# Performance work log

Hardware: AMD Instinct MI355X
Metric: run time of the kernel (lower is better)

## Reference

```python
import jax, jax.numpy as jnp
import numpy as np

EPS = 1e-8


def quaternion_mul(q, m):
    # Hamilton product q * m over last dim of size 4 (w, x, y, z)
    w1, x1, y1, z1 = q[..., 0], q[..., 1], q[..., 2], q[..., 3]
    w2, x2, y2, z2 = m[..., 0], m[..., 1], m[..., 2], m[..., 3]
    return jnp.stack([
        w1 * w2 - x1 * x2 - y1 * y2 - z1 * z2,
        w1 * x2 + x1 * w2 + y1 * z2 - z1 * y2,
        w1 * y2 - x1 * z2 + y1 * w2 + z1 * x2,
        w1 * z2 + x1 * y2 - y1 * x2 + z1 * w2,
    ], axis=-1)


def quaternion_normalize(q):
    n = jnp.linalg.norm(q, axis=-1, keepdims=True)
    return q / (n + EPS)


def setup_inputs() -> dict:
    key = jax.random.key(0)
    k = jax.random.split(key, 5)
    B, S, D, H = 4, 2048, 1024, 1024
    scale = 0.02
    return {
        "x": jax.random.normal(k[0], (B, S, D), dtype=jnp.float32),
        "W_in": jax.random.normal(k[1], (3 * H, D), dtype=jnp.float32) * scale,
        "b_in": jax.random.normal(k[2], (3 * H,), dtype=jnp.float32) * scale,
        "W_out": jax.random.normal(k[3], (D, 4 * H), dtype=jnp.float32) * scale,
        "b_out": jax.random.normal(k[4], (D,), dtype=jnp.float32) * scale,
    }


def reference(x, W_in, b_in, W_out, b_out):
    B, S, D = x.shape
    H = W_in.shape[0] // 3
    # input projection -> rotation parameters v in R^3 per hidden channel
    v = (jnp.einsum('bsd,ed->bse', x, W_in) + b_in).reshape(B, S, H, 3)
    # SU(2) exponential map: v -> unit quaternion
    theta = jnp.linalg.norm(v, axis=-1, keepdims=True)          # (B,S,H,1)
    axis = v / (theta + EPS)
    q_inputs = jnp.concatenate([jnp.cos(theta), jnp.sin(theta) * axis], axis=-1)  # (B,S,H,4)

    # initial identity quaternion state (B,H,4)
    m0 = jnp.zeros((B, H, 4), dtype=x.dtype).at[..., 0].set(1.0)

    def step(m, q_t):
        m_new = quaternion_normalize(quaternion_mul(q_t, m))
        return m_new, m_new

    q_seq = jnp.transpose(q_inputs, (1, 0, 2, 3))               # (S,B,H,4)
    m_final, ms = jax.lax.scan(step, m0, q_seq)                 # ms: (S,B,H,4)

    states = jnp.transpose(ms, (1, 0, 2, 3)).reshape(B, S, 4 * H)
    full_output = jnp.einsum('bsf,df->bsd', states, W_out) + b_out
    return full_output, m_final
```

## Files before the change

kernel.cpp:

```cpp
#include <hip/hip_runtime.h>
#include <hip/hip_bf16.h>
#include <stdint.h>

#define EPSF 1e-8f

typedef __attribute__((ext_vector_type(8))) short short8;
typedef __attribute__((ext_vector_type(8))) _Float16 half8;
typedef __attribute__((ext_vector_type(4))) float floatx4;

__device__ __forceinline__ unsigned short f2h(float f) {
    _Float16 h = (_Float16)f;
    return __builtin_bit_cast(unsigned short, h);
}
__device__ __forceinline__ float h2f(unsigned short u) {
    return (float)__builtin_bit_cast(_Float16, u);
}


__global__ void prep_kernel(const float4* __restrict__ x4, ushort4* __restrict__ x16,
                            const float4* __restrict__ wi4, ushort4* __restrict__ wi16,
                            const float4* __restrict__ wo4, ushort4* __restrict__ wo16,
                            int nx4, int nw4, int nwo4) {
    int i = blockIdx.x * blockDim.x + threadIdx.x;
    float4 f; ushort4 u;
    if (i < nx4) {
        f = x4[i];
        u.x = f2h(f.x); u.y = f2h(f.y); u.z = f2h(f.z); u.w = f2h(f.w);
        x16[i] = u;
    } else if (i < nx4 + nw4) {
        int j = i - nx4;
        f = wi4[j];
        u.x = f2h(f.x); u.y = f2h(f.y); u.z = f2h(f.z); u.w = f2h(f.w);
        wi16[j] = u;
    } else if (i < nx4 + nw4 + nwo4) {
        int j = i - nx4 - nw4;
        f = wo4[j];
        u.x = f2h(f.x); u.y = f2h(f.y); u.z = f2h(f.z); u.w = f2h(f.w);
        wo16[j] = u;
    }
}


__device__ __forceinline__ void gld16(const unsigned short* g, unsigned short* l) {
    __builtin_amdgcn_global_load_lds(
        (const __attribute__((address_space(1))) unsigned int*)g,
        (__attribute__((address_space(3))) unsigned int*)l, 16, 0, 0);
}

template <bool HALFOUT>
__global__ __launch_bounds__(512, 2)
void gemm8p(const unsigned short* __restrict__ Am, const unsigned short* __restrict__ Bm,
            const float* __restrict__ bias, void* __restrict__ Cv,
            int M, int N, int K) {
    constexpr int BM = 256, BN = 128, BK = 64;
    constexpr int ASZ  = BM * BK;
    constexpr int BSZ  = BN * BK;
    constexpr int SLOT = ASZ + BSZ;
    extern __shared__ unsigned short smem[];

    const int tid  = threadIdx.x;
    const int lane = tid & 63;
    const int wid  = tid >> 6;
    const int wr   = wid >> 1;
    const int wc   = wid & 1;
    const int q4   = lane >> 4;
    const int m16  = lane & 15;
    const int x7   = m16 & 7;

    const int nbx = N / BN;
    const int nwg = gridDim.x;
    const int q   = nwg >> 3;
    const int wg  = blockIdx.x;
    const int sz  = (wg & 7) * q + (wg >> 3);
    const int bx  = sz % nbx, by = sz / nbx;
    const int rowA0 = by * BM, rowB0 = bx * BN;

    const int rA = tid >> 3, cA = tid & 7;
    const int cg = cA ^ (rA & 7);
    const unsigned short* srcA = Am + (size_t)(rowA0 + rA) * K + cg * 8;
    const unsigned short* srcB = Bm + (size_t)(rowB0 + rA) * K + cg * 8;
    const int dA = tid * 8;

    int aoffm[4], boffn[4];
#pragma unroll
    for (int m = 0; m < 4; ++m) aoffm[m] = (wr * 64 + m * 16 + m16) * BK;
#pragma unroll
    for (int n = 0; n < 4; ++n) boffn[n] = (wc * 64 + n * 16 + m16) * BK;

    floatx4 acc[4][4];
#pragma unroll
    for (int m = 0; m < 4; ++m)
#pragma unroll
        for (int n = 0; n < 4; ++n)
#pragma unroll
            for (int r = 0; r < 4; ++r) acc[m][n][r] = 0.f;

    const int NT = K / BK;

    auto stageA = [&](int s, int t, int j) {
        gld16(srcA + (size_t)(j * 64) * K + (size_t)t * BK,
              smem + s * SLOT + j * 4096 + dA);
    };
    auto stageB = [&](int s, int t, int j) {
        gld16(srcB + (size_t)(j * 64) * K + (size_t)t * BK,
              smem + s * SLOT + ASZ + j * 4096 + dA);
    };

#pragma unroll
    for (int j = 0; j < 4; ++j) stageA(0, 0, j);
    stageB(0, 0, 0); stageB(0, 0, 1);
#pragma unroll
    for (int j = 0; j < 4; ++j) stageA(1, 1, j);
    stageB(1, 1, 0); stageB(1, 1, 1);

    int s0 = 0;
    for (int t = 0; t < NT; ++t) {
        int s2 = s0 + 2; if (s2 >= 3) s2 -= 3;
        if (t + 1 < NT) asm volatile("s_waitcnt vmcnt(6)" ::: "memory");
        else            asm volatile("s_waitcnt vmcnt(0)" ::: "memory");
        __builtin_amdgcn_s_barrier();
        __builtin_amdgcn_sched_barrier(0);

        const unsigned short* tA = smem + s0 * SLOT;
        const unsigned short* tB = tA + ASZ;

        if (t + 2 < NT) {
#pragma unroll
            for (int j = 0; j < 4; ++j) stageA(s2, t + 2, j);
            stageB(s2, t + 2, 0); stageB(s2, t + 2, 1);
        }

        short8 a0[4], b0[4], a1[4], b1[4];
        {
            const int xo = ((0 + q4) ^ x7) * 8;
#pragma unroll
            for (int m = 0; m < 4; ++m) a0[m] = *(const short8*)(tA + aoffm[m] + xo);
#pragma unroll
            for (int n = 0; n < 4; ++n) b0[n] = *(const short8*)(tB + boffn[n] + xo);
        }
        __builtin_amdgcn_s_setprio(1);
#pragma unroll
        for (int m = 0; m < 4; ++m)
#pragma unroll
            for (int n = 0; n < 4; ++n)
                acc[m][n] = __builtin_amdgcn_mfma_f32_16x16x32_f16(
                    __builtin_bit_cast(half8, a0[m]), __builtin_bit_cast(half8, b0[n]),
                    acc[m][n], 0, 0, 0);
        __builtin_amdgcn_s_setprio(0);

        {
            const int xo = ((4 + q4) ^ x7) * 8;
#pragma unroll
            for (int m = 0; m < 4; ++m) a1[m] = *(const short8*)(tA + aoffm[m] + xo);
#pragma unroll
            for (int n = 0; n < 4; ++n) b1[n] = *(const short8*)(tB + boffn[n] + xo);
        }
        __builtin_amdgcn_s_setprio(1);
#pragma unroll
        for (int m = 0; m < 4; ++m)
#pragma unroll
            for (int n = 0; n < 4; ++n)
                acc[m][n] = __builtin_amdgcn_mfma_f32_16x16x32_f16(
                    __builtin_bit_cast(half8, a1[m]), __builtin_bit_cast(half8, b1[n]),
                    acc[m][n], 0, 0, 0);
        __builtin_amdgcn_s_setprio(0);

        s0 = (s0 + 1 == 3) ? 0 : s0 + 1;
    }

#pragma unroll
    for (int m = 0; m < 4; ++m) {
#pragma unroll
        for (int n = 0; n < 4; ++n) {
            int col  = rowB0 + wc * 64 + n * 16 + m16;
            float bvl = bias[col];
#pragma unroll
            for (int r = 0; r < 4; ++r) {
                int row = rowA0 + wr * 64 + m * 16 + q4 * 4 + r;
                if (HALFOUT)
                    ((unsigned short*)Cv)[(size_t)row * N + col] = f2h(acc[m][n][r] + bvl);
                else
                    ((float*)Cv)[(size_t)row * N + col] = acc[m][n][r] + bvl;
            }
        }
    }
}


struct Q { float w, x, y, z; };

__device__ __forceinline__ Q qmul(Q a, Q b) {
    Q r;
    r.w = a.w * b.w - a.x * b.x - a.y * b.y - a.z * b.z;
    r.x = a.w * b.x + a.x * b.w + a.y * b.z - a.z * b.y;
    r.y = a.w * b.y - a.x * b.z + a.y * b.w + a.z * b.x;
    r.z = a.w * b.z + a.x * b.y - a.y * b.x + a.z * b.w;
    return r;
}
__device__ __forceinline__ Q qnorm(Q a) {
    float nn = a.w * a.w + a.x * a.x + a.y * a.y + a.z * a.z;
    float inv = __frsqrt_rn(nn);
    Q r; r.w = a.w * inv; r.x = a.x * inv; r.y = a.y * inv; r.z = a.z * inv;
    return r;
}
__device__ __forceinline__ Q vquat(float vx, float vy, float vz) {
    float th = sqrtf(vx * vx + vy * vy + vz * vz);
    float s_, c_;
    __sincosf(th, &s_, &c_);
    float k = __fdividef(s_, th + EPSF);
    Q q; q.w = c_; q.x = k * vx; q.y = k * vy; q.z = k * vz;
    return q;
}

#define SEG  64
#define NSEG 32

__global__ __launch_bounds__(256)
void seg_prod_kernel(const unsigned short* __restrict__ v, float* __restrict__ partials,
                     int S, int H) {
    const int b  = blockIdx.z;
    const int h  = blockIdx.y * 64 + (threadIdx.x & 63);
    const int sg = blockIdx.x * 4 + (threadIdx.x >> 6);
    const int s0 = sg * SEG;
    const size_t vstep = (size_t)3 * H;
    const unsigned short* vp = v + ((size_t)b * S + s0) * vstep + (size_t)h * 3;

    constexpr int CH = 8;
    float ax[CH], ay[CH], az[CH], bx[CH], by[CH], bz[CH];
#pragma unroll
    for (int i = 0; i < CH; ++i) {
        ax[i] = h2f(vp[i * vstep + 0]); ay[i] = h2f(vp[i * vstep + 1]); az[i] = h2f(vp[i * vstep + 2]);
    }
    Q c = {1.f, 0.f, 0.f, 0.f};
    const int NC = SEG / CH;
    for (int cc = 0; cc < NC; cc += 2) {
        if (cc + 1 < NC) {
            const unsigned short* p = vp + (size_t)(cc + 1) * CH * vstep;
#pragma unroll
            for (int i = 0; i < CH; ++i) {
                bx[i] = h2f(p[i * vstep + 0]); by[i] = h2f(p[i * vstep + 1]); bz[i] = h2f(p[i * vstep + 2]);
            }
        }
#pragma unroll
        for (int i = 0; i < CH; ++i) c = qmul(vquat(ax[i], ay[i], az[i]), c);
        if (cc + 2 < NC) {
            const unsigned short* p = vp + (size_t)(cc + 2) * CH * vstep;
#pragma unroll
            for (int i = 0; i < CH; ++i) {
                ax[i] = h2f(p[i * vstep + 0]); ay[i] = h2f(p[i * vstep + 1]); az[i] = h2f(p[i * vstep + 2]);
            }
        }
#pragma unroll
        for (int i = 0; i < CH; ++i) c = qmul(vquat(bx[i], by[i], bz[i]), c);
    }
    float4* dst = (float4*)(partials + (((size_t)b * NSEG + sg) * H + h) * 4);
    *dst = make_float4(c.w, c.x, c.y, c.z);
}

__global__ __launch_bounds__(256)
void apply_kernel(const unsigned short* __restrict__ v, const float* __restrict__ partials,
                  unsigned short* __restrict__ st, float* __restrict__ m_final,
                  int S, int H) {
    const int b   = blockIdx.z;
    const int hb  = blockIdx.y * 64;
    const int hl  = threadIdx.x & 63;
    const int h   = hb + hl;
    const int sg  = blockIdx.x * 4 + (threadIdx.x >> 6);
    const int s0  = sg * SEG;
    const size_t vstep = (size_t)3 * H;
    const size_t sstep = (size_t)4 * H;
    const unsigned short* vp = v + ((size_t)b * S + s0) * vstep + (size_t)h * 3;
    unsigned short* sp = st + ((size_t)b * S + s0) * sstep + (size_t)h * 4;

    __shared__ float4 lp[NSEG][64];
    for (int i = threadIdx.x; i < NSEG * 64; i += 256) {
        int s2 = i >> 6, hh = i & 63;
        lp[s2][hh] = *(const float4*)(partials + (((size_t)b * NSEG + s2) * H + hb + hh) * 4);
    }
    __syncthreads();

    Q R = {1.f, 0.f, 0.f, 0.f};
    for (int s2 = 0; s2 < sg; ++s2) {
        float4 pv = lp[s2][hl];
        Q pq = {pv.x, pv.y, pv.z, pv.w};
        R = qmul(pq, R);
    }

    constexpr int CH = 8;
    float ax[CH], ay[CH], az[CH], bx[CH], by[CH], bz[CH];
#pragma unroll
    for (int i = 0; i < CH; ++i) {
        ax[i] = h2f(vp[i * vstep + 0]); ay[i] = h2f(vp[i * vstep + 1]); az[i] = h2f(vp[i * vstep + 2]);
    }
    const int NC = SEG / CH;
    for (int cc = 0; cc < NC; cc += 2) {
        if (cc + 1 < NC) {
            const unsigned short* pp = vp + (size_t)(cc + 1) * CH * vstep;
#pragma unroll
            for (int i = 0; i < CH; ++i) {
                bx[i] = h2f(pp[i * vstep + 0]); by[i] = h2f(pp[i * vstep + 1]); bz[i] = h2f(pp[i * vstep + 2]);
            }
        }
#pragma unroll
        for (int i = 0; i < CH; ++i) {
            R = qmul(vquat(ax[i], ay[i], az[i]), R);
            Q m = qnorm(R);
            ushort4 u; u.x = f2h(m.w); u.y = f2h(m.x); u.z = f2h(m.y); u.w = f2h(m.z);
            *(ushort4*)(sp + (size_t)(cc * CH + i) * sstep) = u;
        }
        if (cc + 2 < NC) {
            const unsigned short* pp = vp + (size_t)(cc + 2) * CH * vstep;
#pragma unroll
            for (int i = 0; i < CH; ++i) {
                ax[i] = h2f(pp[i * vstep + 0]); ay[i] = h2f(pp[i * vstep + 1]); az[i] = h2f(pp[i * vstep + 2]);
            }
        }
#pragma unroll
        for (int i = 0; i < CH; ++i) {
            R = qmul(vquat(bx[i], by[i], bz[i]), R);
            Q m = qnorm(R);
            ushort4 u; u.x = f2h(m.w); u.y = f2h(m.x); u.z = f2h(m.y); u.w = f2h(m.z);
            *(ushort4*)(sp + (size_t)((cc + 1) * CH + i) * sstep) = u;
        }
    }

    if (sg == NSEG - 1) {
        Q m = qnorm(R);
        float* mf = m_final + ((size_t)b * H + h) * 4;
        mf[0] = m.w; mf[1] = m.x; mf[2] = m.y; mf[3] = m.z;
    }
}


extern "C" void kernel_launch(void* const* d_in, const int* in_sizes, int n_in,
                              void* d_out, int out_size, void* d_ws, size_t ws_size,
                              hipStream_t stream) {
    const float* x     = (const float*)d_in[0];
    const float* W_in  = (const float*)d_in[1];
    const float* b_in  = (const float*)d_in[2];
    const float* W_out = (const float*)d_in[3];
    const float* b_out = (const float*)d_in[4];
    float* out = (float*)d_out;

    const int B = 4, S = 2048, D = 1024, H = 1024;
    const int M  = B * S;
    const int N1 = 3 * H;
    const int K1 = D;
    const int N2 = D;
    const int K2 = 4 * H;

    char* ws = (char*)d_ws;
    unsigned short* v    = (unsigned short*)(ws);
    unsigned short* st   = (unsigned short*)(ws + 50331648u);
    unsigned short* x16  = (unsigned short*)(ws + 50331648u);
    unsigned short* wi16 = (unsigned short*)(ws + 50331648u + 16777216u);
    unsigned short* wo16 = (unsigned short*)(ws + 117440512u);

    float* partials = out;

    const int nx  = M * K1;
    const int nw  = N1 * K1;
    const int nwo = N2 * K2;
    const int n4  = (nx + nw + nwo) / 4;

    constexpr int LDSB = 147456;
    static int attr_done = 0;
    if (!attr_done) {
        hipFuncSetAttribute(reinterpret_cast<const void*>(&gemm8p<true>),
                            hipFuncAttributeMaxDynamicSharedMemorySize, LDSB);
        hipFuncSetAttribute(reinterpret_cast<const void*>(&gemm8p<false>),
                            hipFuncAttributeMaxDynamicSharedMemorySize, LDSB);
        attr_done = 1;
    }

    prep_kernel<<<(n4 + 255) / 256, 256, 0, stream>>>(
        (const float4*)x, (ushort4*)x16, (const float4*)W_in, (ushort4*)wi16,
        (const float4*)W_out, (ushort4*)wo16, nx / 4, nw / 4, nwo / 4);

    gemm8p<true><<<dim3((M / 256) * (N1 / 128)), 512, LDSB, stream>>>(
        x16, wi16, b_in, v, M, N1, K1);

    dim3 sg_grid(NSEG / 4, H / 64, B);
    seg_prod_kernel<<<sg_grid, 256, 0, stream>>>(v, partials, S, H);
    apply_kernel<<<sg_grid, 256, 0, stream>>>(v, partials, st, out + (size_t)M * D, S, H);

    gemm8p<false><<<dim3((M / 256) * (N2 / 128)), 512, LDSB, stream>>>(
        st, wo16, b_out, out, M, N2, K2);
}
```

Measured before the change: 297.4 us.

## Switch GEMM to 32x32x16 MFMA with software-pipelined LDS fragment reads

Replaces the 16x16x32 MFMA tiling (4x4 accumulators per wave) with 32x32x16 MFMA instructions (2x2 accumulators of 16 floats). The main loop is restructured so LDS fragment reads for the next k-slice, including the first slice of the next tile, are issued before the MFMAs on the current slice. The barrier/waitcnt placement moves to mid-iteration to allow this prefetch. The aim is fewer LDS reads per FLOP and better overlap of LDS latency with matrix math. The cost is more complex synchronisation and a different output row mapping in the epilogue.

```diff
diff --git a/kernel.cpp b/kernel.cpp
--- a/kernel.cpp
+++ b/kernel.cpp
@@ -6,7 +6,7 @@
 
 typedef __attribute__((ext_vector_type(8))) short short8;
 typedef __attribute__((ext_vector_type(8))) _Float16 half8;
-typedef __attribute__((ext_vector_type(4))) float floatx4;
+typedef __attribute__((ext_vector_type(16))) float floatx16;
 
 __device__ __forceinline__ unsigned short f2h(float f) {
     _Float16 h = (_Float16)f;
@@ -63,9 +63,9 @@
     const int wid  = tid >> 6;
     const int wr   = wid >> 1;
     const int wc   = wid & 1;
-    const int q4   = lane >> 4;
-    const int m16  = lane & 15;
-    const int x7   = m16 & 7;
+    const int m32  = lane & 31;
+    const int half = lane >> 5;
+    const int x7   = m32 & 7;
 
     const int nbx = N / BN;
     const int nwg = gridDim.x;
@@ -81,19 +81,19 @@
     const unsigned short* srcB = Bm + (size_t)(rowB0 + rA) * K + cg * 8;
     const int dA = tid * 8;
 
-    int aoffm[4], boffn[4];
-#pragma unroll
-    for (int m = 0; m < 4; ++m) aoffm[m] = (wr * 64 + m * 16 + m16) * BK;
-#pragma unroll
-    for (int n = 0; n < 4; ++n) boffn[n] = (wc * 64 + n * 16 + m16) * BK;
-
-    floatx4 acc[4][4];
-#pragma unroll
-    for (int m = 0; m < 4; ++m)
-#pragma unroll
-        for (int n = 0; n < 4; ++n)
-#pragma unroll
-            for (int r = 0; r < 4; ++r) acc[m][n][r] = 0.f;
+    int aoff[2], boff[2];
+#pragma unroll
+    for (int m = 0; m < 2; ++m) aoff[m] = (wr * 64 + m * 32 + m32) * BK;
+#pragma unroll
+    for (int n = 0; n < 2; ++n) boff[n] = (wc * 64 + n * 32 + m32) * BK;
+
+    floatx16 acc[2][2];
+#pragma unroll
+    for (int m = 0; m < 2; ++m)
+#pragma unroll
+        for (int n = 0; n < 2; ++n)
+#pragma unroll
+            for (int r = 0; r < 16; ++r) acc[m][n][r] = 0.f;
 
     const int NT = K / BK;
 
@@ -106,6 +106,26 @@
               smem + s * SLOT + ASZ + j * 4096 + dA);
     };
 
+    auto RD = [&](const unsigned short* tA, const unsigned short* tB, int ks,
+                  short8* Ra, short8* Rb) {
+        const int xo = (((ks * 2 + half)) ^ x7) * 8;
+#pragma unroll
+        for (int m = 0; m < 2; ++m) Ra[m] = *(const short8*)(tA + aoff[m] + xo);
+#pragma unroll
+        for (int n = 0; n < 2; ++n) Rb[n] = *(const short8*)(tB + boff[n] + xo);
+    };
+    auto MM = [&](short8* Ra, short8* Rb) {
+        __builtin_amdgcn_s_setprio(1);
+#pragma unroll
+        for (int m = 0; m < 2; ++m)
+#pragma unroll
+            for (int n = 0; n < 2; ++n)
+                acc[m][n] = __builtin_amdgcn_mfma_f32_32x32x16_f16(
+                    __builtin_bit_cast(half8, Ra[m]), __builtin_bit_cast(half8, Rb[n]),
+                    acc[m][n], 0, 0, 0);
+        __builtin_amdgcn_s_setprio(0);
+    };
+
 #pragma unroll
     for (int j = 0; j < 4; ++j) stageA(0, 0, j);
     stageB(0, 0, 0); stageB(0, 0, 1);
@@ -113,70 +133,58 @@
     for (int j = 0; j < 4; ++j) stageA(1, 1, j);
     stageB(1, 1, 0); stageB(1, 1, 1);
 
+    asm volatile("s_waitcnt vmcnt(6)" ::: "memory");
+    __builtin_amdgcn_s_barrier();
+    __builtin_amdgcn_sched_barrier(0);
+
+    short8 RA0[2], RB0[2], RA1[2], RB1[2];
+    RD(smem, smem + ASZ, 0, RA0, RB0);
+
     int s0 = 0;
     for (int t = 0; t < NT; ++t) {
-        int s2 = s0 + 2; if (s2 >= 3) s2 -= 3;
-        if (t + 1 < NT) asm volatile("s_waitcnt vmcnt(6)" ::: "memory");
+        __builtin_amdgcn_s_barrier();
+        __builtin_amdgcn_sched_barrier(0);
+
+        int s1 = s0 + 1; if (s1 == 3) s1 = 0;
+        int s2 = s1 + 1; if (s2 == 3) s2 = 0;
+        const unsigned short* tA  = smem + s0 * SLOT;
+        const unsigned short* tB  = tA + ASZ;
+        const unsigned short* tA1 = smem + s1 * SLOT;
+        const unsigned short* tB1 = tA1 + ASZ;
+
+        if (t + 2 < NT) {
+#pragma unroll
+            for (int j = 0; j < 4; ++j) stageA(s2, t + 2, j);
+            stageB(s2, t + 2, 0); stageB(s2, t + 2, 1);
+        }
+
+        RD(tA, tB, 1, RA1, RB1);
+        MM(RA0, RB0);
+        RD(tA, tB, 2, RA0, RB0);
+        MM(RA1, RB1);
+
+        if (t + 2 < NT) asm volatile("s_waitcnt vmcnt(6)" ::: "memory");
         else            asm volatile("s_waitcnt vmcnt(0)" ::: "memory");
         __builtin_amdgcn_s_barrier();
         __builtin_amdgcn_sched_barrier(0);
 
-        const unsigned short* tA = smem + s0 * SLOT;
-        const unsigned short* tB = tA + ASZ;
-
-        if (t + 2 < NT) {
-#pragma unroll
-            for (int j = 0; j < 4; ++j) stageA(s2, t + 2, j);
-            stageB(s2, t + 2, 0); stageB(s2, t + 2, 1);
-        }
-
-        short8 a0[4], b0[4], a1[4], b1[4];
-        {
-            const int xo = ((0 + q4) ^ x7) * 8;
-#pragma unroll
-            for (int m = 0; m < 4; ++m) a0[m] = *(const short8*)(tA + aoffm[m] + xo);
-#pragma unroll
-            for (int n = 0; n < 4; ++n) b0[n] = *(const short8*)(tB + boffn[n] + xo);
-        }
-        __builtin_amdgcn_s_setprio(1);
-#pragma unroll
-        for (int m = 0; m < 4; ++m)
-#pragma unroll
-            for (int n = 0; n < 4; ++n)
-                acc[m][n] = __builtin_amdgcn_mfma_f32_16x16x32_f16(
-                    __builtin_bit_cast(half8, a0[m]), __builtin_bit_cast(half8, b0[n]),
-                    acc[m][n], 0, 0, 0);
-        __builtin_amdgcn_s_setprio(0);
-
-        {
-            const int xo = ((4 + q4) ^ x7) * 8;
-#pragma unroll
-            for (int m = 0; m < 4; ++m) a1[m] = *(const short8*)(tA + aoffm[m] + xo);
-#pragma unroll
-            for (int n = 0; n < 4; ++n) b1[n] = *(const short8*)(tB + boffn[n] + xo);
-        }
-        __builtin_amdgcn_s_setprio(1);
-#pragma unroll
-        for (int m = 0; m < 4; ++m)
-#pragma unroll
-            for (int n = 0; n < 4; ++n)
-                acc[m][n] = __builtin_amdgcn_mfma_f32_16x16x32_f16(
-                    __builtin_bit_cast(half8, a1[m]), __builtin_bit_cast(half8, b1[n]),
-                    acc[m][n], 0, 0, 0);
-        __builtin_amdgcn_s_setprio(0);
-
-        s0 = (s0 + 1 == 3) ? 0 : s0 + 1;
-    }
-
-#pragma unroll
-    for (int m = 0; m < 4; ++m) {
-#pragma unroll
-        for (int n = 0; n < 4; ++n) {
-            int col  = rowB0 + wc * 64 + n * 16 + m16;
+        RD(tA, tB, 3, RA1, RB1);
+        MM(RA0, RB0);
+        if (t + 1 < NT) RD(tA1, tB1, 0, RA0, RB0);
+        MM(RA1, RB1);
+
+        s0 = s1;
+    }
+
+#pragma unroll
+    for (int m = 0; m < 2; ++m) {
+#pragma unroll
+        for (int n = 0; n < 2; ++n) {
+            int col  = rowB0 + wc * 64 + n * 32 + m32;
             float bvl = bias[col];
 #pragma unroll
-            for (int r = 0; r < 4; ++r) {
-                int row = rowA0 + wr * 64 + m * 16 + q4 * 4 + r;
+            for (int r = 0; r < 16; ++r) {
+                int row = rowA0 + wr * 64 + m * 32 + (r & 3) + 8 * (r >> 2) + 4 * half;
                 if (HALFOUT)
                     ((unsigned short*)Cv)[(size_t)row * N + col] = f2h(acc[m][n][r] + bvl);
                 else
```

Measured after the change: 312.5 us. 1.05x slower.
